# Performance work log

Hardware: AMD Instinct MI355X
Metric: run time of the kernel (lower is better)

Reference implementation:

```python
import jax, jax.numpy as jnp
import numpy as np

NUM_USER = 1_000_000
NUM_ITEM = 100_000
HIDDEN = 64
NUM_PAIRS = 2_000_000


def setup_inputs() -> dict:
    key = jax.random.key(0)
    k1, k2, k3, k4 = jax.random.split(key, 4)
    user_emb = jax.random.normal(k1, (NUM_USER, HIDDEN), dtype=jnp.float32)
    item_emb = jax.random.normal(k2, (NUM_ITEM, HIDDEN), dtype=jnp.float32)
    user_ids = jax.random.randint(k3, (NUM_PAIRS,), 0, NUM_USER, dtype=jnp.int32)
    item_ids = jax.random.randint(k4, (NUM_PAIRS,), 0, NUM_ITEM, dtype=jnp.int32)
    return {"user_emb": user_emb, "item_emb": item_emb,
            "user_ids": user_ids, "item_ids": item_ids}


def reference(user_emb, item_emb, user_ids, item_ids):
    # PMF rating prediction: relu(<U[u], V[i]>) for each observed (u, i) pair.
    u = user_emb[user_ids]          # [P, D] gather
    v = item_emb[item_ids]          # [P, D] gather
    ratings = jnp.einsum('pd,pd->p', u, v)  # per-pair dot product
    return jax.nn.relu(ratings)
```

## Files before the change

### kernel.cpp

```cpp
#include <hip/hip_runtime.h>


constexpr int HIDDEN = 64;
constexpr int K = 4;

__global__ __launch_bounds__(256) void pmf_dot_kernel(
    const float* __restrict__ user_emb,
    const float* __restrict__ item_emb,
    const int*   __restrict__ user_ids,
    const int*   __restrict__ item_ids,
    float*       __restrict__ out,
    int n_pairs)
{
    const int group  = (blockIdx.x * blockDim.x + threadIdx.x) >> 4;
    const int lane16 = threadIdx.x & 15;
    const int p0     = group * K;

    if (p0 + K <= n_pairs) {
        const int4 u4 = *reinterpret_cast<const int4*>(user_ids + p0);
        const int4 i4 = *reinterpret_cast<const int4*>(item_ids + p0);

        const float4* up0 = reinterpret_cast<const float4*>(user_emb + (size_t)u4.x * HIDDEN) + lane16;
        const float4* up1 = reinterpret_cast<const float4*>(user_emb + (size_t)u4.y * HIDDEN) + lane16;
        const float4* up2 = reinterpret_cast<const float4*>(user_emb + (size_t)u4.z * HIDDEN) + lane16;
        const float4* up3 = reinterpret_cast<const float4*>(user_emb + (size_t)u4.w * HIDDEN) + lane16;
        const float4* vp0 = reinterpret_cast<const float4*>(item_emb + (size_t)i4.x * HIDDEN) + lane16;
        const float4* vp1 = reinterpret_cast<const float4*>(item_emb + (size_t)i4.y * HIDDEN) + lane16;
        const float4* vp2 = reinterpret_cast<const float4*>(item_emb + (size_t)i4.z * HIDDEN) + lane16;
        const float4* vp3 = reinterpret_cast<const float4*>(item_emb + (size_t)i4.w * HIDDEN) + lane16;

        const float4 a0 = *up0, a1 = *up1, a2 = *up2, a3 = *up3;
        const float4 b0 = *vp0, b1 = *vp1, b2 = *vp2, b3 = *vp3;

        float d0 = a0.x * b0.x + a0.y * b0.y + a0.z * b0.z + a0.w * b0.w;
        float d1 = a1.x * b1.x + a1.y * b1.y + a1.z * b1.z + a1.w * b1.w;
        float d2 = a2.x * b2.x + a2.y * b2.y + a2.z * b2.z + a2.w * b2.w;
        float d3 = a3.x * b3.x + a3.y * b3.y + a3.z * b3.z + a3.w * b3.w;

        #pragma unroll
        for (int s = 1; s < 16; s <<= 1) {
            d0 += __shfl_xor(d0, s, 16);
            d1 += __shfl_xor(d1, s, 16);
            d2 += __shfl_xor(d2, s, 16);
            d3 += __shfl_xor(d3, s, 16);
        }

        if (lane16 == 0) {
            float4 r;
            r.x = d0 > 0.0f ? d0 : 0.0f;
            r.y = d1 > 0.0f ? d1 : 0.0f;
            r.z = d2 > 0.0f ? d2 : 0.0f;
            r.w = d3 > 0.0f ? d3 : 0.0f;
            *reinterpret_cast<float4*>(out + p0) = r;
        }
    } else if (p0 < n_pairs) {
        for (int p = p0; p < n_pairs; ++p) {
            const int uid = user_ids[p];
            const int iid = item_ids[p];
            const float4 a = *(reinterpret_cast<const float4*>(user_emb + (size_t)uid * HIDDEN) + lane16);
            const float4 b = *(reinterpret_cast<const float4*>(item_emb + (size_t)iid * HIDDEN) + lane16);
            float d = a.x * b.x + a.y * b.y + a.z * b.z + a.w * b.w;
            #pragma unroll
            for (int s = 1; s < 16; s <<= 1) d += __shfl_xor(d, s, 16);
            if (lane16 == 0) out[p] = d > 0.0f ? d : 0.0f;
        }
    }
}

extern "C" void kernel_launch(void* const* d_in, const int* in_sizes, int n_in,
                              void* d_out, int out_size, void* d_ws, size_t ws_size,
                              hipStream_t stream) {
    const float* user_emb = (const float*)d_in[0];
    const float* item_emb = (const float*)d_in[1];
    const int*   user_ids = (const int*)d_in[2];
    const int*   item_ids = (const int*)d_in[3];
    float* out = (float*)d_out;

    const int n_pairs = in_sizes[2];
    const int threads = 256;
    const int pairs_per_block = (threads / 16) * K;
    const int blocks = (n_pairs + pairs_per_block - 1) / pairs_per_block;

    pmf_dot_kernel<<<blocks, threads, 0, stream>>>(
        user_emb, item_emb, user_ids, item_ids, out, n_pairs);
}
```

Baseline: 419.4 us.

## Bucket pairs by user id range before gathering to improve locality

Adds a histogram, a single-block scan, and an atomic scatter that group pairs into 4096 buckets by user id, then runs the dot kernel over the sorted pairs and writes results back through a position array. The aim is for user-embedding gathers within a bucket to hit nearby rows, improving cache locality over the 256MB user table. In exchange it adds extra kernel launches, atomics, roughly 24MB of extra index traffic and scattered output writes. The old direct path is kept as a fallback when the workspace is too small.

```diff
diff --git a/kernel.cpp b/kernel.cpp
--- a/kernel.cpp
+++ b/kernel.cpp
@@ -2,40 +2,88 @@
 
 
 constexpr int HIDDEN = 64;
-constexpr int K = 4;
-
-__global__ __launch_bounds__(256) void pmf_dot_kernel(
-    const float* __restrict__ user_emb,
-    const float* __restrict__ item_emb,
-    const int*   __restrict__ user_ids,
-    const int*   __restrict__ item_ids,
-    float*       __restrict__ out,
-    int n_pairs)
+constexpr int K      = 4;
+constexpr int NB     = 4096;
+constexpr int BSHIFT = 8;
+
+__device__ __forceinline__ float dot16(const float4& a, const float4& b) {
+    return a.x * b.x + a.y * b.y + a.z * b.z + a.w * b.w;
+}
+
+__global__ __launch_bounds__(256) void hist_kernel(
+    const int* __restrict__ user_ids, int* __restrict__ hist, int n)
+{
+    int p = blockIdx.x * blockDim.x + threadIdx.x;
+    if (p < n) atomicAdd(&hist[user_ids[p] >> BSHIFT], 1);
+}
+
+__global__ __launch_bounds__(1024) void scan_kernel(
+    const int* __restrict__ hist, int* __restrict__ offs)
+{
+    __shared__ int part[1024];
+    const int t = threadIdx.x;
+    int4 h = reinterpret_cast<const int4*>(hist)[t];
+    int s = h.x + h.y + h.z + h.w;
+    part[t] = s;
+    __syncthreads();
+    #pragma unroll
+    for (int d = 1; d < 1024; d <<= 1) {
+        int v = (t >= d) ? part[t - d] : 0;
+        __syncthreads();
+        part[t] += v;
+        __syncthreads();
+    }
+    int excl = part[t] - s;
+    int4 o;
+    o.x = excl;
+    o.y = o.x + h.x;
+    o.z = o.y + h.y;
+    o.w = o.z + h.z;
+    reinterpret_cast<int4*>(offs)[t] = o;
+}
+
+__global__ __launch_bounds__(256) void scatter_kernel(
+    const int* __restrict__ user_ids, const int* __restrict__ item_ids,
+    int* __restrict__ offs, int* __restrict__ uid_s, int* __restrict__ iid_s,
+    int* __restrict__ pos_s, int n)
+{
+    int p = blockIdx.x * blockDim.x + threadIdx.x;
+    if (p < n) {
+        int u = user_ids[p];
+        int q = atomicAdd(&offs[u >> BSHIFT], 1);
+        uid_s[q] = u;
+        iid_s[q] = item_ids[p];
+        pos_s[q] = p;
+    }
+}
+
+__global__ __launch_bounds__(256) void pmf_dot_bucketed(
+    const float* __restrict__ user_emb, const float* __restrict__ item_emb,
+    const int* __restrict__ uid_s, const int* __restrict__ iid_s,
+    const int* __restrict__ pos_s, float* __restrict__ out, int n)
 {
     const int group  = (blockIdx.x * blockDim.x + threadIdx.x) >> 4;
     const int lane16 = threadIdx.x & 15;
-    const int p0     = group * K;
-
-    if (p0 + K <= n_pairs) {
-        const int4 u4 = *reinterpret_cast<const int4*>(user_ids + p0);
-        const int4 i4 = *reinterpret_cast<const int4*>(item_ids + p0);
-
-        const float4* up0 = reinterpret_cast<const float4*>(user_emb + (size_t)u4.x * HIDDEN) + lane16;
-        const float4* up1 = reinterpret_cast<const float4*>(user_emb + (size_t)u4.y * HIDDEN) + lane16;
-        const float4* up2 = reinterpret_cast<const float4*>(user_emb + (size_t)u4.z * HIDDEN) + lane16;
-        const float4* up3 = reinterpret_cast<const float4*>(user_emb + (size_t)u4.w * HIDDEN) + lane16;
-        const float4* vp0 = reinterpret_cast<const float4*>(item_emb + (size_t)i4.x * HIDDEN) + lane16;
-        const float4* vp1 = reinterpret_cast<const float4*>(item_emb + (size_t)i4.y * HIDDEN) + lane16;
-        const float4* vp2 = reinterpret_cast<const float4*>(item_emb + (size_t)i4.z * HIDDEN) + lane16;
-        const float4* vp3 = reinterpret_cast<const float4*>(item_emb + (size_t)i4.w * HIDDEN) + lane16;
-
-        const float4 a0 = *up0, a1 = *up1, a2 = *up2, a3 = *up3;
-        const float4 b0 = *vp0, b1 = *vp1, b2 = *vp2, b3 = *vp3;
-
-        float d0 = a0.x * b0.x + a0.y * b0.y + a0.z * b0.z + a0.w * b0.w;
-        float d1 = a1.x * b1.x + a1.y * b1.y + a1.z * b1.z + a1.w * b1.w;
-        float d2 = a2.x * b2.x + a2.y * b2.y + a2.z * b2.z + a2.w * b2.w;
-        float d3 = a3.x * b3.x + a3.y * b3.y + a3.z * b3.z + a3.w * b3.w;
+    const int q0     = group * K;
+
+    if (q0 + K <= n) {
+        const int4 u4 = *reinterpret_cast<const int4*>(uid_s + q0);
+        const int4 i4 = *reinterpret_cast<const int4*>(iid_s + q0);
+        const int4 p4 = *reinterpret_cast<const int4*>(pos_s + q0);
+
+        const float4 a0 = *(reinterpret_cast<const float4*>(user_emb + (size_t)u4.x * HIDDEN) + lane16);
+        const float4 a1 = *(reinterpret_cast<const float4*>(user_emb + (size_t)u4.y * HIDDEN) + lane16);
+        const float4 a2 = *(reinterpret_cast<const float4*>(user_emb + (size_t)u4.z * HIDDEN) + lane16);
+        const float4 a3 = *(reinterpret_cast<const float4*>(user_emb + (size_t)u4.w * HIDDEN) + lane16);
+        const float4 b0 = *(reinterpret_cast<const float4*>(item_emb + (size_t)i4.x * HIDDEN) + lane16);
+        const float4 b1 = *(reinterpret_cast<const float4*>(item_emb + (size_t)i4.y * HIDDEN) + lane16);
+        const float4 b2 = *(reinterpret_cast<const float4*>(item_emb + (size_t)i4.z * HIDDEN) + lane16);
+        const float4 b3 = *(reinterpret_cast<const float4*>(item_emb + (size_t)i4.w * HIDDEN) + lane16);
+
+        float d0 = dot16(a0, b0);
+        float d1 = dot16(a1, b1);
+        float d2 = dot16(a2, b2);
+        float d3 = dot16(a3, b3);
 
         #pragma unroll
         for (int s = 1; s < 16; s <<= 1) {
@@ -46,20 +94,65 @@
         }
 
         if (lane16 == 0) {
-            float4 r;
-            r.x = d0 > 0.0f ? d0 : 0.0f;
-            r.y = d1 > 0.0f ? d1 : 0.0f;
-            r.z = d2 > 0.0f ? d2 : 0.0f;
-            r.w = d3 > 0.0f ? d3 : 0.0f;
+            out[p4.x] = d0 > 0.0f ? d0 : 0.0f;
+            out[p4.y] = d1 > 0.0f ? d1 : 0.0f;
+            out[p4.z] = d2 > 0.0f ? d2 : 0.0f;
+            out[p4.w] = d3 > 0.0f ? d3 : 0.0f;
+        }
+    } else if (q0 < n) {
+        for (int q = q0; q < n; ++q) {
+            const int uid = uid_s[q];
+            const int iid = iid_s[q];
+            const float4 a = *(reinterpret_cast<const float4*>(user_emb + (size_t)uid * HIDDEN) + lane16);
+            const float4 b = *(reinterpret_cast<const float4*>(item_emb + (size_t)iid * HIDDEN) + lane16);
+            float d = dot16(a, b);
+            #pragma unroll
+            for (int s = 1; s < 16; s <<= 1) d += __shfl_xor(d, s, 16);
+            if (lane16 == 0) out[pos_s[q]] = d > 0.0f ? d : 0.0f;
+        }
+    }
+}
+
+__global__ __launch_bounds__(256) void pmf_dot_direct(
+    const float* __restrict__ user_emb, const float* __restrict__ item_emb,
+    const int* __restrict__ user_ids, const int* __restrict__ item_ids,
+    float* __restrict__ out, int n)
+{
+    const int group  = (blockIdx.x * blockDim.x + threadIdx.x) >> 4;
+    const int lane16 = threadIdx.x & 15;
+    const int p0     = group * K;
+
+    if (p0 + K <= n) {
+        const int4 u4 = *reinterpret_cast<const int4*>(user_ids + p0);
+        const int4 i4 = *reinterpret_cast<const int4*>(item_ids + p0);
+        const float4 a0 = *(reinterpret_cast<const float4*>(user_emb + (size_t)u4.x * HIDDEN) + lane16);
+        const float4 a1 = *(reinterpret_cast<const float4*>(user_emb + (size_t)u4.y * HIDDEN) + lane16);
+        const float4 a2 = *(reinterpret_cast<const float4*>(user_emb + (size_t)u4.z * HIDDEN) + lane16);
+        const float4 a3 = *(reinterpret_cast<const float4*>(user_emb + (size_t)u4.w * HIDDEN) + lane16);
+        const float4 b0 = *(reinterpret_cast<const float4*>(item_emb + (size_t)i4.x * HIDDEN) + lane16);
+        const float4 b1 = *(reinterpret_cast<const float4*>(item_emb + (size_t)i4.y * HIDDEN) + lane16);
+        const float4 b2 = *(reinterpret_cast<const float4*>(item_emb + (size_t)i4.z * HIDDEN) + lane16);
+        const float4 b3 = *(reinterpret_cast<const float4*>(item_emb + (size_t)i4.w * HIDDEN) + lane16);
+        float d0 = dot16(a0, b0), d1 = dot16(a1, b1), d2 = dot16(a2, b2), d3 = dot16(a3, b3);
+        #pragma unroll
+        for (int s = 1; s < 16; s <<= 1) {
+            d0 += __shfl_xor(d0, s, 16);
+            d1 += __shfl_xor(d1, s, 16);
+            d2 += __shfl_xor(d2, s, 16);
+            d3 += __shfl_xor(d3, s, 16);
+        }
+        if (lane16 == 0) {
+            float4 r = { d0 > 0.0f ? d0 : 0.0f, d1 > 0.0f ? d1 : 0.0f,
+                         d2 > 0.0f ? d2 : 0.0f, d3 > 0.0f ? d3 : 0.0f };
             *reinterpret_cast<float4*>(out + p0) = r;
         }
-    } else if (p0 < n_pairs) {
-        for (int p = p0; p < n_pairs; ++p) {
+    } else if (p0 < n) {
+        for (int p = p0; p < n; ++p) {
             const int uid = user_ids[p];
             const int iid = item_ids[p];
             const float4 a = *(reinterpret_cast<const float4*>(user_emb + (size_t)uid * HIDDEN) + lane16);
             const float4 b = *(reinterpret_cast<const float4*>(item_emb + (size_t)iid * HIDDEN) + lane16);
-            float d = a.x * b.x + a.y * b.y + a.z * b.z + a.w * b.w;
+            float d = dot16(a, b);
             #pragma unroll
             for (int s = 1; s < 16; s <<= 1) d += __shfl_xor(d, s, 16);
             if (lane16 == 0) out[p] = d > 0.0f ? d : 0.0f;
@@ -76,11 +169,35 @@
     const int*   item_ids = (const int*)d_in[3];
     float* out = (float*)d_out;
 
-    const int n_pairs = in_sizes[2];
+    const int n = in_sizes[2];
+
+    const size_t histB = (size_t)NB * 4;
+    const size_t base  = 2 * histB;
+    const size_t need  = base + 3 * (size_t)n * 4;
+
     const int threads = 256;
     const int pairs_per_block = (threads / 16) * K;
-    const int blocks = (n_pairs + pairs_per_block - 1) / pairs_per_block;
-
-    pmf_dot_kernel<<<blocks, threads, 0, stream>>>(
-        user_emb, item_emb, user_ids, item_ids, out, n_pairs);
-}
+    const int dot_blocks = (n + pairs_per_block - 1) / pairs_per_block;
+
+    if (ws_size >= need) {
+        char* ws    = (char*)d_ws;
+        int*  hist  = (int*)(ws);
+        int*  offs  = (int*)(ws + histB);
+        int*  uid_s = (int*)(ws + base);
+        int*  iid_s = (int*)(ws + base + (size_t)n * 4);
+        int*  pos_s = (int*)(ws + base + 2 * (size_t)n * 4);
+
+        hipMemsetAsync(hist, 0, histB, stream);
+
+        const int lin_blocks = (n + threads - 1) / threads;
+        hist_kernel<<<lin_blocks, threads, 0, stream>>>(user_ids, hist, n);
+        scan_kernel<<<1, 1024, 0, stream>>>(hist, offs);
+        scatter_kernel<<<lin_blocks, threads, 0, stream>>>(
+            user_ids, item_ids, offs, uid_s, iid_s, pos_s, n);
+        pmf_dot_bucketed<<<dot_blocks, threads, 0, stream>>>(
+            user_emb, item_emb, uid_s, iid_s, pos_s, out, n);
+    } else {
+        pmf_dot_direct<<<dot_blocks, threads, 0, stream>>>(
+            user_emb, item_emb, user_ids, item_ids, out, n);
+    }
+}
```

Measured after the change: 712.1 us. +69.8%, slower.
